# Optimization experiments

Hardware: AMD Instinct MI355X
Metric: run time of the kernel (lower is better)

## Reference

```python
import jax, jax.numpy as jnp
import numpy as np

TOPK = 32
N_HEADS = 8
NEG_INF = float('-inf')


def _l2norm(x, axis):
    # torch F.normalize(p=2): x / max(||x||, 1e-12)
    n = jnp.sqrt(jnp.sum(x * x, axis=axis, keepdims=True))
    return x / jnp.maximum(n, 1e-12)


def _topk_attention(q_in, k_in, v_in, Wq, bq, Wk, bk, Wv, bv):
    # shared ExactTopKAttention (dropout = identity in eval)
    N, L, Hd = q_in.shape
    S = k_in.shape[1]
    E = Hd // N_HEADS
    q = (q_in @ Wq + bq).reshape(N, L, N_HEADS, E)
    k = (k_in @ Wk + bk).reshape(N, S, N_HEADS, E)
    v = (v_in @ Wv + bv).reshape(N, S, N_HEADS, E)
    QK = jnp.einsum('nlhe,nshe->nhls', q, k)  # [N,H,L,S]
    kk = min(TOPK, S)
    _, idx = jax.lax.top_k(QK, kk)  # [N,H,L,kk]
    ni = jnp.arange(N)[:, None, None, None]
    hi = jnp.arange(N_HEADS)[None, :, None, None]
    li = jnp.arange(L)[None, None, :, None]
    mask = jnp.full(QK.shape, NEG_INF, QK.dtype).at[ni, hi, li, idx].set(0.0)
    temp = 1.0 / np.sqrt(E)
    A = jax.nn.softmax(temp * (QK + mask), axis=-1)
    V = jnp.einsum('nhls,nshd->nlhd', A, v).reshape(N, L, Hd)
    return V, A


def _attention_pool(x, w_pool, b_pool):
    # softmax-weighted pooling over sequence dim
    logits = jnp.einsum('bld,d->bl', x, w_pool) + b_pool
    a = jax.nn.softmax(logits, axis=-1)
    pooled = jnp.einsum('bl,bld->bd', a, x)
    return pooled, a


def setup_inputs() -> dict:
    key = jax.random.key(0)
    ks = jax.random.split(key, 16)
    B, L, S, H = 16, 2048, 128, 512
    s = 0.02
    return {
        'seqs_emb': jax.random.normal(ks[0], (B, L, H), jnp.float32),
        'smiles_emb': jax.random.normal(ks[1], (B, S, H), jnp.float32),
        'Wq': jax.random.normal(ks[2], (H, H), jnp.float32) * s,
        'bq': jax.random.normal(ks[3], (H,), jnp.float32) * s,
        'Wk': jax.random.normal(ks[4], (H, H), jnp.float32) * s,
        'bk': jax.random.normal(ks[5], (H,), jnp.float32) * s,
        'Wv': jax.random.normal(ks[6], (H, H), jnp.float32) * s,
        'bv': jax.random.normal(ks[7], (H,), jnp.float32) * s,
        'w_pool': jax.random.normal(ks[8], (H,), jnp.float32) * s,
        'b_pool': jnp.zeros((), jnp.float32),
        'W1': jax.random.normal(ks[9], (2 * H, 2 * H), jnp.float32) * s,
        'b1': jax.random.normal(ks[10], (2 * H,), jnp.float32) * s,
        'W2': jax.random.normal(ks[11], (2 * H, H), jnp.float32) * s,
        'b2': jax.random.normal(ks[12], (H,), jnp.float32) * s,
        'W3': jax.random.normal(ks[13], (H, 1), jnp.float32) * s,
        'b3': jnp.zeros((1,), jnp.float32),
    }


def reference(seqs_emb, smiles_emb, Wq, bq, Wk, bk, Wv, bv, w_pool, b_pool,
              W1, b1, W2, b2, W3, b3):
    # F.normalize(..., dim=1): normalize over the sequence dimension (faithful)
    seqs = _l2norm(seqs_emb, axis=1)
    smis = _l2norm(smiles_emb, axis=1)
    # fusion 1: queries = protein, keys/values = drug (shared weights)
    smiles_out, _ = _topk_attention(seqs, smis, smis, Wq, bq, Wk, bk, Wv, bv)
    smiles_pooled, smiles_attn_pool = _attention_pool(smiles_out, w_pool, b_pool)
    # fusion 2: queries = drug, keys/values = protein (same weights)
    seqs_out, _ = _topk_attention(smis, seqs, seqs, Wq, bq, Wk, bk, Wv, bv)
    seqs_pooled, seqs_attn_pool = _attention_pool(seqs_out, w_pool, b_pool)
    emb = jnp.concatenate([smiles_pooled, seqs_pooled], axis=1)
    emb = _l2norm(emb, axis=1)
    h = jax.nn.relu(emb @ W1 + b1)
    h = jax.nn.relu(h @ W2 + b2)
    out = (h @ W3 + b3).squeeze(-1)  # task_type='reg': no sigmoid
    return emb, out, smiles_attn_pool, seqs_attn_pool
```

## Files before the change

### kernel.cpp

```cpp
#include <hip/hip_runtime.h>
#include <cfloat>
#include <cstdint>

#define NC 1536

#define OUT_EMB 0
#define OUT_OUT 16384
#define OUT_A1  16400
#define OUT_A2  49168

#define WS_NRM_S   0u
#define WS_NRM_M   32768u
#define WS_BCAT    360448u
#define WS_LOG1    366592u
#define WS_PP1     505856u
#define WS_EMB     800768u
#define WS_H1      866304u
#define WS_H2      931840u
#define WS_WCT     1048576u
#define WS_SMISNB  2621440u
#define WS_PSMIS   4718592u
#define WS_SEQSOUT 11010048u
#define WS_SEQSNB  15204352u
#define WS_PSEQS   48758784u
#define WS_SMILOUT WS_SEQSNB
#define WS_PART    WS_PSEQS
#define WS_PARTM   (WS_PSEQS + 2097152u)

typedef float f32x4 __attribute__((ext_vector_type(4)));
typedef __bf16 bf16x8 __attribute__((ext_vector_type(8)));
typedef unsigned short u16x8 __attribute__((ext_vector_type(8)));

__device__ __forceinline__ float bf2f(unsigned short h) {
  return __uint_as_float(((unsigned int)h) << 16);
}
__device__ __forceinline__ unsigned short f2bf(float f) {
  unsigned int u = __float_as_uint(f);
  return (unsigned short)((u + 0x7FFFu + ((u >> 16) & 1u)) >> 16);
}
__device__ __forceinline__ void gld16(const unsigned short* g, unsigned short* l) {
  __builtin_amdgcn_global_load_lds(
      (__attribute__((address_space(1))) unsigned int*)(uintptr_t)g,
      (__attribute__((address_space(3))) unsigned int*)l, 16, 0, 0);
}

__device__ __forceinline__ unsigned pos2elem(unsigned m) {
  unsigned lo = __brev(m & 0xFFFFu) >> 16;
  unsigned hi = __brev(m >> 16) >> 16;
  lo = (lo | (lo << 8)) & 0x00FF00FFu;
  lo = (lo | (lo << 4)) & 0x0F0F0F0Fu;
  lo = (lo | (lo << 2)) & 0x33333333u;
  lo = (lo | (lo << 1)) & 0x55555555u;
  hi = (hi | (hi << 8)) & 0x00FF00FFu;
  hi = (hi | (hi << 4)) & 0x0F0F0F0Fu;
  hi = (hi | (hi << 2)) & 0x33333333u;
  hi = (hi | (hi << 1)) & 0x55555555u;
  return lo | (hi << 1);
}

#define TRANSPOSE16(B)                                                                             \
  {                                                                                                \
    unsigned t;                                                                                    \
    t = (B[0] ^ (B[8] >> 8)) & 0x00FF00FFu; B[0] ^= t; B[8] ^= (t << 8);                           \
    t = (B[1] ^ (B[9] >> 8)) & 0x00FF00FFu; B[1] ^= t; B[9] ^= (t << 8);                           \
    t = (B[2] ^ (B[10] >> 8)) & 0x00FF00FFu; B[2] ^= t; B[10] ^= (t << 8);                         \
    t = (B[3] ^ (B[11] >> 8)) & 0x00FF00FFu; B[3] ^= t; B[11] ^= (t << 8);                         \
    t = (B[4] ^ (B[12] >> 8)) & 0x00FF00FFu; B[4] ^= t; B[12] ^= (t << 8);                         \
    t = (B[5] ^ (B[13] >> 8)) & 0x00FF00FFu; B[5] ^= t; B[13] ^= (t << 8);                         \
    t = (B[6] ^ (B[14] >> 8)) & 0x00FF00FFu; B[6] ^= t; B[14] ^= (t << 8);                         \
    t = (B[7] ^ (B[15] >> 8)) & 0x00FF00FFu; B[7] ^= t; B[15] ^= (t << 8);                         \
    t = (B[0] ^ (B[4] >> 4)) & 0x0F0F0F0Fu; B[0] ^= t; B[4] ^= (t << 4);                           \
    t = (B[1] ^ (B[5] >> 4)) & 0x0F0F0F0Fu; B[1] ^= t; B[5] ^= (t << 4);                           \
    t = (B[2] ^ (B[6] >> 4)) & 0x0F0F0F0Fu; B[2] ^= t; B[6] ^= (t << 4);                           \
    t = (B[3] ^ (B[7] >> 4)) & 0x0F0F0F0Fu; B[3] ^= t; B[7] ^= (t << 4);                           \
    t = (B[8] ^ (B[12] >> 4)) & 0x0F0F0F0Fu; B[8] ^= t; B[12] ^= (t << 4);                         \
    t = (B[9] ^ (B[13] >> 4)) & 0x0F0F0F0Fu; B[9] ^= t; B[13] ^= (t << 4);                         \
    t = (B[10] ^ (B[14] >> 4)) & 0x0F0F0F0Fu; B[10] ^= t; B[14] ^= (t << 4);                       \
    t = (B[11] ^ (B[15] >> 4)) & 0x0F0F0F0Fu; B[11] ^= t; B[15] ^= (t << 4);                       \
    t = (B[0] ^ (B[2] >> 2)) & 0x33333333u; B[0] ^= t; B[2] ^= (t << 2);                           \
    t = (B[1] ^ (B[3] >> 2)) & 0x33333333u; B[1] ^= t; B[3] ^= (t << 2);                           \
    t = (B[4] ^ (B[6] >> 2)) & 0x33333333u; B[4] ^= t; B[6] ^= (t << 2);                           \
    t = (B[5] ^ (B[7] >> 2)) & 0x33333333u; B[5] ^= t; B[7] ^= (t << 2);                           \
    t = (B[8] ^ (B[10] >> 2)) & 0x33333333u; B[8] ^= t; B[10] ^= (t << 2);                         \
    t = (B[9] ^ (B[11] >> 2)) & 0x33333333u; B[9] ^= t; B[11] ^= (t << 2);                         \
    t = (B[12] ^ (B[14] >> 2)) & 0x33333333u; B[12] ^= t; B[14] ^= (t << 2);                       \
    t = (B[13] ^ (B[15] >> 2)) & 0x33333333u; B[13] ^= t; B[15] ^= (t << 2);                       \
    t = (B[0] ^ (B[1] >> 1)) & 0x55555555u; B[0] ^= t; B[1] ^= (t << 1);                           \
    t = (B[2] ^ (B[3] >> 1)) & 0x55555555u; B[2] ^= t; B[3] ^= (t << 1);                           \
    t = (B[4] ^ (B[5] >> 1)) & 0x55555555u; B[4] ^= t; B[5] ^= (t << 1);                           \
    t = (B[6] ^ (B[7] >> 1)) & 0x55555555u; B[6] ^= t; B[7] ^= (t << 1);                           \
    t = (B[8] ^ (B[9] >> 1)) & 0x55555555u; B[8] ^= t; B[9] ^= (t << 1);                           \
    t = (B[10] ^ (B[11] >> 1)) & 0x55555555u; B[10] ^= t; B[11] ^= (t << 1);                       \
    t = (B[12] ^ (B[13] >> 1)) & 0x55555555u; B[12] ^= t; B[13] ^= (t << 1);                       \
    t = (B[14] ^ (B[15] >> 1)) & 0x55555555u; B[14] ^= t; B[15] ^= (t << 1);                       \
  }

__global__ __launch_bounds__(128) void knorm_part(const float* __restrict__ seqs, const float* __restrict__ smis,
                                                  float* __restrict__ part_s, float* __restrict__ part_m) {
  int ls = blockIdx.x, b = blockIdx.y, t = threadIdx.x;
  const float* x; float* part; int slab;
  if (ls < 64) { x = seqs; part = part_s + (size_t)(b * 64 + ls) * 512; slab = b * 64 + ls; }
  else { x = smis; part = part_m + (size_t)(b * 4 + (ls - 64)) * 512; slab = b * 4 + (ls - 64); }
  const float* xp = x + (size_t)slab * 32 * 512 + t * 4;
  float ax = 0.f, ay = 0.f, az = 0.f, aw = 0.f;
  for (int l = 0; l < 32; ++l) {
    float4 v = *(const float4*)(xp + (size_t)l * 512);
    ax += v.x * v.x; ay += v.y * v.y; az += v.z * v.z; aw += v.w * v.w;
  }
  float4 r = {ax, ay, az, aw};
  *(float4*)(part + t * 4) = r;
}

__global__ __launch_bounds__(256) void kfinprep(const float* __restrict__ part_s, const float* __restrict__ part_m,
                                                float* __restrict__ nrm_s, float* __restrict__ nrm_m,
                                                const float* __restrict__ Wq, const float* __restrict__ Wk,
                                                const float* __restrict__ Wv, unsigned short* __restrict__ WT,
                                                const float* bq, const float* bk, const float* bv,
                                                float* bcat, float* log1, float* h1pre, float* h2pre) {
  __shared__ float T[32][33];
  int t = threadIdx.x;
  if (blockIdx.x < 64) {
    int bh0 = blockIdx.x;
    const float* part; float* inv; int NS, bh;
    if (bh0 < 32) { part = part_s; inv = nrm_s; NS = 64; bh = bh0; }
    else { part = part_m; inv = nrm_m; NS = 4; bh = bh0 - 32; }
    int b = bh >> 1, col = (bh & 1) * 256 + t;
    float s = 0.f;
    for (int j = 0; j < NS; ++j) s += part[((size_t)(b * NS + j)) * 512 + col];
    inv[(size_t)b * 512 + col] = 1.f / fmaxf(sqrtf(s), 1e-12f);
  } else {
    int id = blockIdx.x - 64;
    int m = id >> 8, r256 = id & 255;
    if (m < 3) {
      int ti = r256 >> 4, tj = r256 & 15;
      const float* W = m == 0 ? Wq : (m == 1 ? Wk : Wv);
      int c = t & 31, r0 = t >> 5;
#pragma unroll
      for (int j = 0; j < 4; ++j) {
        int r = r0 + j * 8;
        T[r][c] = W[(size_t)(ti * 32 + r) * 512 + tj * 32 + c];
      }
      __syncthreads();
#pragma unroll
      for (int j = 0; j < 4; ++j) {
        int r = r0 + j * 8;
        WT[(size_t)(m * 512 + tj * 32 + r) * 512 + ti * 32 + c] = f2bf(T[c][r]);
      }
    } else {
      int i = r256 * 256 + t;
      if (i < 1536) bcat[i] = i < 512 ? bq[i] : (i < 1024 ? bk[i - 512] : bv[i - 1024]);
      else if (i < 34304) log1[i - 1536] = 0.f;
      else if (i < 50688) h1pre[i - 34304] = 0.f;
      else if (i < 58880) h2pre[i - 50688] = 0.f;
    }
  }
}

__global__ __launch_bounds__(256) void kcast(const float* __restrict__ seqs, const float* __restrict__ smis,
                                             const float* __restrict__ nrm_s, const float* __restrict__ nrm_m,
                                             unsigned short* __restrict__ seqs_nb, unsigned short* __restrict__ smis_nb) {
  const float* x; const float* inv; unsigned short* o; int i4, shiftB;
  if (blockIdx.x < 16384) {
    i4 = (blockIdx.x * 256 + threadIdx.x) * 4; x = seqs; inv = nrm_s; o = seqs_nb; shiftB = 20;
  } else {
    i4 = ((blockIdx.x - 16384) * 256 + threadIdx.x) * 4; x = smis; inv = nrm_m; o = smis_nb; shiftB = 16;
  }
  int b = i4 >> shiftB;
  float4 v = *(const float4*)(x + i4);
  float4 nv = *(const float4*)(inv + (b << 9) + (i4 & 511));
  ushort4 r;
  r.x = f2bf(v.x * nv.x); r.y = f2bf(v.y * nv.y);
  r.z = f2bf(v.z * nv.z); r.w = f2bf(v.w * nv.w);
  *(ushort4*)(o + i4) = r;
}

__global__ __launch_bounds__(256) void kgemm(const unsigned short* __restrict__ A1,
                                             const unsigned short* __restrict__ A2,
                                             const unsigned short* __restrict__ Bt,
                                             const float* __restrict__ bias,
                                             unsigned short* __restrict__ C1,
                                             unsigned short* __restrict__ C2) {
  const int K = 512, N = NC, NT = 12;
  __shared__ unsigned short As[2][128 * 32], Bs[2][128 * 32];
  int tid = threadIdx.x, lane = tid & 63, wave = tid >> 6;
  int id = blockIdx.x;
  const unsigned short* A; unsigned short* C;
  if (id < 3072) { A = A1; C = C1; }
  else { A = A2; C = C2; id -= 3072; }
  int xcd = id & 7, j = id >> 3;
  int mloc = j / NT, n = j - mloc * NT;
  int m0 = (mloc * 8 + xcd) * 128, n0 = n * 128;
  f32x4 acc[4][4] = {};
  int wm = (wave >> 1) * 64, wn = (wave & 1) * 64;
  int frow = lane & 15, fk = (lane >> 4) * 8;

  auto stage = [&](int buf, int k0) {
#pragma unroll
    for (int jj = 0; jj < 2; ++jj) {
      int ch = jj * 256 + tid;
      int row = ch >> 2, kc = (ch & 3) * 8;
      gld16(A + (size_t)(m0 + row) * K + k0 + kc, As[buf] + ch * 8);
      gld16(Bt + (size_t)(n0 + row) * K + k0 + kc, Bs[buf] + ch * 8);
    }
  };

  stage(0, 0);
  __syncthreads();
  int nk = K >> 5;
  for (int it = 0; it < nk; ++it) {
    int cur = it & 1;
    if (it + 1 < nk) stage(cur ^ 1, (it + 1) << 5);
    bf16x8 af[4], bfv[4];
#pragma unroll
    for (int mt = 0; mt < 4; ++mt) af[mt] = *(const bf16x8*)&As[cur][(wm + mt * 16 + frow) * 32 + fk];
#pragma unroll
    for (int nt = 0; nt < 4; ++nt) bfv[nt] = *(const bf16x8*)&Bs[cur][(wn + nt * 16 + frow) * 32 + fk];
#pragma unroll
    for (int mt = 0; mt < 4; ++mt)
#pragma unroll
      for (int nt = 0; nt < 4; ++nt)
        acc[mt][nt] = __builtin_amdgcn_mfma_f32_16x16x32_bf16(af[mt], bfv[nt], acc[mt][nt], 0, 0, 0);
    __syncthreads();
  }
  int q = lane >> 4, c15 = lane & 15;
#pragma unroll
  for (int mt = 0; mt < 4; ++mt)
#pragma unroll
    for (int nt = 0; nt < 4; ++nt) {
      int col = n0 + wn + nt * 16 + c15;
      float bv = bias[col];
#pragma unroll
      for (int r = 0; r < 4; ++r) {
        int row = m0 + wm + mt * 16 + q * 4 + r;
        C[(size_t)row * N + col] = f2bf(acc[mt][nt][r] + bv);
      }
    }
}

__global__ __launch_bounds__(256) void kfusion1(const unsigned short* __restrict__ Pseqs,
                                                const unsigned short* __restrict__ Psmis,
                                                const float* __restrict__ wp,
                                                unsigned short* __restrict__ smil,
                                                float* __restrict__ logits) {
  constexpr int PP = 136;
  __shared__ unsigned short Sc[64 * PP];
  __shared__ unsigned short Vt[64 * PP];
  int tid = threadIdx.x, lane = tid & 63, w = tid >> 6;
  int lt = blockIdx.x, h = blockIdx.y, b = blockIdx.z;
  int l0 = lt * 64;
  int frow = lane & 15, q = lane >> 4, fk8 = q * 8;

  for (int ch = tid; ch < 1024; ch += 256) {
    int s = ch >> 3, e8 = (ch & 7) * 8;
    u16x8 vv = *(const u16x8*)&Psmis[(size_t)(b * 128 + s) * NC + 1024 + h * 64 + e8];
#pragma unroll
    for (int j = 0; j < 8; ++j) {
      int e = e8 + j;
      Vt[e * PP + (s ^ (e & 56))] = vv[j];
    }
  }

  {
    f32x4 acc[8] = {};
    const unsigned short* qrow = Pseqs + (size_t)(b * 2048 + l0 + w * 16 + frow) * NC + h * 64 + fk8;
#pragma unroll
    for (int ks = 0; ks < 2; ++ks) {
      bf16x8 a = *(const bf16x8*)(qrow + ks * 32);
#pragma unroll
      for (int nt = 0; nt < 8; ++nt) {
        bf16x8 bb = *(const bf16x8*)&Psmis[(size_t)(b * 128 + nt * 16 + frow) * NC + 512 + h * 64 + ks * 32 + fk8];
        acc[nt] = __builtin_amdgcn_mfma_f32_16x16x32_bf16(a, bb, acc[nt], 0, 0, 0);
      }
    }
#pragma unroll
    for (int nt = 0; nt < 8; ++nt)
#pragma unroll
      for (int r = 0; r < 4; ++r)
        Sc[(w * 16 + q * 4 + r) * PP + nt * 16 + frow] = f2bf(acc[nt][r]);
  }
  __syncthreads();

  {
    int i = lane >> 2, seg = lane & 3;
    int row = w * 16 + i;
    unsigned short* rb = &Sc[row * PP + seg * 32];
    unsigned orig[16], B[16];
#pragma unroll
    for (int jb = 0; jb < 4; ++jb) {
      uint4 qv = *(const uint4*)(rb + jb * 8);
      orig[jb * 4 + 0] = qv.x; orig[jb * 4 + 1] = qv.y;
      orig[jb * 4 + 2] = qv.z; orig[jb * 4 + 3] = qv.w;
    }
#pragma unroll
    for (int j = 0; j < 16; ++j) {
      unsigned s = (orig[j] >> 15) & 0x00010001u;
      B[j] = orig[j] ^ (s * 0x7FFFu) ^ 0x80008000u;
    }
    TRANSPOSE16(B)
    unsigned act = 0xFFFFFFFFu, gt = 0u, Tv = 0u;
    int rem = 32;
#pragma unroll
    for (int bit = 15; bit >= 0; --bit) {
      unsigned bm = B[15 - bit] & act;
      int c = __popc(bm);
      c += __shfl_xor(c, 1);
      c += __shfl_xor(c, 2);
      bool take = (c >= rem);
      act = take ? bm : (act ^ bm);
      gt = take ? gt : (gt | bm);
      rem = take ? rem : (rem - c);
      Tv = take ? (Tv | (1u << bit)) : Tv;
    }
    unsigned hT = (Tv & 0x8000u) ? (Tv ^ 0x8000u) : (Tv ^ 0xFFFFu);
    float vT = bf2f((unsigned short)hT);
    unsigned gtE = pos2elem(gt), actE = pos2elem(act);
    int pc = __popc(actE);
    int pr1 = __shfl_up(pc, 1);
    int inc = pc + ((seg >= 1) ? pr1 : 0);
    int pr2 = __shfl_up(inc, 2);
    inc += ((seg >= 2) ? pr2 : 0);
    int tie_pre = inc - pc;
    int budget = rem - tie_pre;
    budget = budget < 0 ? 0 : (budget > pc ? pc : budget);
    unsigned selT = 0u, m = actE;
    for (int t = 0; t < budget; ++t) { unsigned bb2 = m & (~m + 1u); selT |= bb2; m ^= bb2; }
    unsigned sel = gtE | selT;
    unsigned* wb = (unsigned*)rb;
#pragma unroll
    for (int j = 0; j < 16; ++j) {
      unsigned d = orig[j];
      float v0 = bf2f((unsigned short)(d & 0xFFFFu));
      float v1 = bf2f((unsigned short)(d >> 16));
      float e0 = ((sel >> (2 * j)) & 1u) ? __expf((v0 - vT) * 0.125f) : 0.f;
      float e1 = ((sel >> (2 * j + 1)) & 1u) ? __expf((v1 - vT) * 0.125f) : 0.f;
      wb[j] = (unsigned)f2bf(e0) | ((unsigned)f2bf(e1) << 16);
    }
  }
  __syncthreads();

  f32x4 oacc[4] = {};
  f32x4 dacc = {};
  bf16x8 ones;
#pragma unroll
  for (int j = 0; j < 8; ++j) ones[j] = (__bf16)1.0f;
#pragma unroll
  for (int k0 = 0; k0 < 128; k0 += 32) {
    bf16x8 a = *(const bf16x8*)&Sc[(w * 16 + frow) * PP + k0 + fk8];
#pragma unroll
    for (int nt = 0; nt < 4; ++nt) {
      int e = nt * 16 + frow;
      bf16x8 bb = *(const bf16x8*)&Vt[e * PP + ((k0 + fk8) ^ (e & 56))];
      oacc[nt] = __builtin_amdgcn_mfma_f32_16x16x32_bf16(a, bb, oacc[nt], 0, 0, 0);
    }
    dacc = __builtin_amdgcn_mfma_f32_16x16x32_bf16(a, ones, dacc, 0, 0, 0);
  }
  float inv4[4];
#pragma unroll
  for (int r = 0; r < 4; ++r) inv4[r] = 1.f / dacc[r];
  float wv[4];
#pragma unroll
  for (int nt = 0; nt < 4; ++nt) wv[nt] = wp[h * 64 + nt * 16 + frow];
  float lg[4];
#pragma unroll
  for (int r = 0; r < 4; ++r) lg[r] = 0.f;
#pragma unroll
  for (int nt = 0; nt < 4; ++nt)
#pragma unroll
    for (int r = 0; r < 4; ++r) {
      float ov = oacc[nt][r] * inv4[r];
      smil[(size_t)(b * 2048 + l0 + w * 16 + q * 4 + r) * 512 + h * 64 + nt * 16 + frow] = f2bf(ov);
      lg[r] += ov * wv[nt];
    }
#pragma unroll
  for (int d = 1; d < 16; d <<= 1)
#pragma unroll
    for (int r = 0; r < 4; ++r) lg[r] += __shfl_xor(lg[r], d);
  if (frow == 0) {
#pragma unroll
    for (int r = 0; r < 4; ++r)
      atomicAdd(&logits[b * 2048 + l0 + w * 16 + q * 4 + r], lg[r]);
  }
}

__global__ __launch_bounds__(1024, 8) void kf2fused(const unsigned short* __restrict__ Psmis,
                                                    const unsigned short* __restrict__ Pseqs,
                                                    float* __restrict__ seqs_out) {
  __shared__ unsigned short S[16 * 2048];
  __shared__ float pS[16][32];
  __shared__ int   sS[16][32];
  int tid = threadIdx.x, lane = tid & 63, w = tid >> 6;
  int bh = blockIdx.x, rt = blockIdx.y;
  int b = bh >> 3, h = bh & 7;
  int frow = lane & 15, q = lane >> 4, fk8 = q * 8;

  {
    const unsigned short* qrow = Psmis + (size_t)(b * 128 + rt * 16 + frow) * NC + h * 64 + fk8;
    bf16x8 a0 = *(const bf16x8*)qrow;
    bf16x8 a1 = *(const bf16x8*)(qrow + 32);
    const unsigned short* Bb = Pseqs + (size_t)(b * 2048) * NC + 512 + h * 64 + fk8;
#pragma unroll
    for (int nt = 0; nt < 8; ++nt) {
      int n0 = w * 128 + nt * 16;
      const unsigned short* brow = Bb + (size_t)(n0 + frow) * NC;
      bf16x8 b0 = *(const bf16x8*)brow;
      bf16x8 b1 = *(const bf16x8*)(brow + 32);
      f32x4 acc = {};
      acc = __builtin_amdgcn_mfma_f32_16x16x32_bf16(a0, b0, acc, 0, 0, 0);
      acc = __builtin_amdgcn_mfma_f32_16x16x32_bf16(a1, b1, acc, 0, 0, 0);
      int el = n0 + frow;
      int cc = el >> 3;
      int base = cc ^ ((cc >> 3) & 7);
#pragma unroll
      for (int r = 0; r < 4; ++r) {
        int row = q * 4 + r;
        S[row * 2048 + ((base ^ (row & 7)) << 3) + (el & 7)] = f2bf(acc[r]);
      }
    }
  }
  __syncthreads();

  int lr = w, x = w & 7;

  unsigned B[16];
  {
    const uint4* p4 = (const uint4*)&S[lr * 2048];
#pragma unroll
    for (int i = 0; i < 4; ++i) {
      int cc = lane * 4 + i;
      int base = cc ^ ((cc >> 3) & 7);
      uint4 qa = p4[base ^ x];
      B[i * 4 + 0] = qa.x; B[i * 4 + 1] = qa.y; B[i * 4 + 2] = qa.z; B[i * 4 + 3] = qa.w;
    }
  }
#pragma unroll
  for (int i = 0; i < 16; ++i) {
    unsigned s0 = (B[i] >> 15) & 0x00010001u;
    B[i] = B[i] ^ (s0 * 0x7FFFu) ^ 0x80008000u;
  }
  TRANSPOSE16(B)
  unsigned act = 0xFFFFFFFFu, gt = 0u, Tv = 0u;
  int rem = 32;
#pragma unroll
  for (int bit = 15; bit >= 0; --bit) {
    unsigned bm = B[15 - bit] & act;
    int c = __popc(bm);
#pragma unroll
    for (int d = 1; d < 64; d <<= 1) c += __shfl_xor(c, d);
    bool take = (c >= rem);
    unsigned actx = act ^ bm;
    act = take ? bm : actx;
    gt = take ? gt : (gt | bm);
    rem = take ? rem : (rem - c);
    Tv = take ? (Tv | (1u << bit)) : Tv;
  }
  unsigned hT = (Tv & 0x8000u) ? (Tv ^ 0x8000u) : (Tv ^ 0xFFFFu);
  float vT = bf2f((unsigned short)hT);

  gt = pos2elem(gt);
  act = pos2elem(act);

  int pc_tie = __popc(act);
  int inc = pc_tie;
#pragma unroll
  for (int d = 1; d < 64; d <<= 1) { int y = __shfl_up(inc, d); if (lane >= d) inc += y; }
  int tie_pre = inc - pc_tie;
  int budget = rem - tie_pre;
  budget = budget < 0 ? 0 : (budget > pc_tie ? pc_tie : budget);
  int total_lane = __popc(gt) + budget;
  int inc2 = total_lane;
#pragma unroll
  for (int d = 1; d < 64; d <<= 1) { int y = __shfl_up(inc2, d); if (lane >= d) inc2 += y; }
  int slot = inc2 - total_lane;

  float lsum = 0.f;
  {
    unsigned m = gt;
    while (m) {
      int e = __builtin_ctz(m); m &= m - 1;
      int gidx = (lane << 5) + e;
      int cc = gidx >> 3;
      float v = bf2f(S[lr * 2048 + (((cc ^ ((cc >> 3) & 7)) ^ x) << 3) + (gidx & 7)]);
      float ev = __expf((v - vT) * 0.125f);
      pS[lr][slot] = ev; sS[lr][slot] = gidx; ++slot; lsum += ev;
    }
    m = act;
    for (int taken = 0; taken < budget; ++taken) {
      int e = __builtin_ctz(m); m &= m - 1;
      int gidx = (lane << 5) + e;
      int cc = gidx >> 3;
      float v = bf2f(S[lr * 2048 + (((cc ^ ((cc >> 3) & 7)) ^ x) << 3) + (gidx & 7)]);
      float ev = __expf((v - vT) * 0.125f);
      pS[lr][slot] = ev; sS[lr][slot] = gidx; ++slot; lsum += ev;
    }
  }
  float den = lsum;
#pragma unroll
  for (int d = 1; d < 64; d <<= 1) den += __shfl_xor(den, d);

  float acc = 0.f;
  const unsigned short* Vb = Pseqs + (size_t)(b * 2048) * NC + 1024 + h * 64 + lane;
#pragma unroll 8
  for (int t = 0; t < 32; ++t) {
    acc += pS[lr][t] * bf2f(Vb[(size_t)sS[lr][t] * NC]);
  }
  seqs_out[(size_t)(b * 128 + rt * 16 + lr) * 512 + h * 64 + lane] = acc / den;
}

__global__ __launch_bounds__(256) void kpool1b(const unsigned short* __restrict__ x,
                                               const float* __restrict__ logits,
                                               float* __restrict__ aout, float* __restrict__ pp) {
  __shared__ float red[256];
  __shared__ float aS[256];
  int t = threadIdx.x;
  int b = blockIdx.x >> 4, ls = (blockIdx.x >> 1) & 7, cj = blockIdx.x & 1;
  const float* lg = logits + b * 2048;
  float lm = -FLT_MAX;
  for (int j = t; j < 2048; j += 256) lm = fmaxf(lm, lg[j]);
  red[t] = lm; __syncthreads();
  for (int s = 128; s > 0; s >>= 1) { if (t < s) red[t] = fmaxf(red[t], red[t + s]); __syncthreads(); }
  float M = red[0]; __syncthreads();
  float sm = 0.f;
  for (int j = t; j < 2048; j += 256) sm += __expf(lg[j] - M);
  red[t] = sm; __syncthreads();
  for (int s = 128; s > 0; s >>= 1) { if (t < s) red[t] += red[t + s]; __syncthreads(); }
  float D = red[0];
  int l0 = ls * 256;
  float a = __expf(lg[l0 + t] - M) / D;
  aS[t] = a;
  if (cj == 0) aout[b * 2048 + l0 + t] = a;
  __syncthreads();
  int col = cj * 256 + t;
  float acc0 = 0.f;
  const unsigned short* xb = x + ((size_t)b * 2048 + l0) * 512 + col;
#pragma unroll 8
  for (int ll = 0; ll < 256; ++ll) acc0 += aS[ll] * bf2f(xb[(size_t)ll * 512]);
  pp[(size_t)(b * 8 + ls) * 512 + col] = acc0;
}

__global__ __launch_bounds__(256) void kpool2emb(const float* __restrict__ x,
                                                 const float* __restrict__ wp, const float* __restrict__ bp,
                                                 const float* __restrict__ pp,
                                                 float* __restrict__ a2out, float* __restrict__ embo) {
  __shared__ float lgS[128];
  __shared__ float red[256];
  int t = threadIdx.x, lane = t & 63, wave = t >> 6;
  int b = blockIdx.x;
  for (int i = 0; i < 32; ++i) {
    int row = wave * 32 + i;
    const float* xp = x + (size_t)(b * 128 + row) * 512;
    float acc = 0.f;
#pragma unroll
    for (int j = 0; j < 8; ++j) acc += xp[lane + 64 * j] * wp[lane + 64 * j];
#pragma unroll
    for (int d = 1; d < 64; d <<= 1) acc += __shfl_xor(acc, d);
    if (lane == 0) lgS[row] = acc + bp[0];
  }
  __syncthreads();
  if (wave == 0) {
    float a0 = lgS[lane], a1 = lgS[64 + lane];
    float m = fmaxf(a0, a1);
#pragma unroll
    for (int d = 1; d < 64; d <<= 1) m = fmaxf(m, __shfl_xor(m, d));
    float e0 = __expf(a0 - m), e1 = __expf(a1 - m);
    float sden = e0 + e1;
#pragma unroll
    for (int d = 1; d < 64; d <<= 1) sden += __shfl_xor(sden, d);
    a0 = e0 / sden; a1 = e1 / sden;
    lgS[lane] = a0; lgS[64 + lane] = a1;
    a2out[b * 128 + lane] = a0;
    a2out[b * 128 + 64 + lane] = a1;
  }
  __syncthreads();
  float acc0 = 0.f, acc1 = 0.f;
#pragma unroll 4
  for (int row = 0; row < 128; ++row) {
    float av = lgS[row];
    const float* xp = x + (size_t)(b * 128 + row) * 512;
    acc0 += av * xp[t];
    acc1 += av * xp[t + 256];
  }
  float pre0 = 0.f, pre1 = 0.f;
  for (int lsl = 0; lsl < 8; ++lsl) {
    pre0 += pp[(size_t)(b * 8 + lsl) * 512 + t];
    pre1 += pp[(size_t)(b * 8 + lsl) * 512 + 256 + t];
  }
  float ssq = pre0 * pre0 + pre1 * pre1 + acc0 * acc0 + acc1 * acc1;
  red[t] = ssq; __syncthreads();
  for (int s2 = 128; s2 > 0; s2 >>= 1) { if (t < s2) red[t] += red[t + s2]; __syncthreads(); }
  float inv = 1.f / fmaxf(sqrtf(red[0]), 1e-12f);
  embo[(size_t)b * 1024 + t] = pre0 * inv;
  embo[(size_t)b * 1024 + 256 + t] = pre1 * inv;
  embo[(size_t)b * 1024 + 512 + t] = acc0 * inv;
  embo[(size_t)b * 1024 + 768 + t] = acc1 * inv;
}

__global__ __launch_bounds__(256) void kh1(const float* __restrict__ emb, const float* __restrict__ W1,
                                           float* __restrict__ h1pre) {
  __shared__ float eS[4][64];
  int t = threadIdx.x;
  int jc = blockIdx.x, bg = blockIdx.y, kc = blockIdx.z;
  int j = jc * 256 + t, b0 = bg * 4, i0 = kc * 64;
  eS[t >> 6][t & 63] = emb[(size_t)(b0 + (t >> 6)) * 1024 + i0 + (t & 63)];
  __syncthreads();
  float a0 = 0.f, a1 = 0.f, a2 = 0.f, a3 = 0.f;
#pragma unroll 8
  for (int i = 0; i < 64; ++i) {
    float w = W1[(size_t)(i0 + i) * 1024 + j];
    a0 += eS[0][i] * w; a1 += eS[1][i] * w; a2 += eS[2][i] * w; a3 += eS[3][i] * w;
  }
  atomicAdd(&h1pre[(b0 + 0) * 1024 + j], a0);
  atomicAdd(&h1pre[(b0 + 1) * 1024 + j], a1);
  atomicAdd(&h1pre[(b0 + 2) * 1024 + j], a2);
  atomicAdd(&h1pre[(b0 + 3) * 1024 + j], a3);
}

__global__ __launch_bounds__(256) void kh2(const float* __restrict__ h1pre, const float* __restrict__ b1,
                                           const float* __restrict__ W2, float* __restrict__ h2pre) {
  __shared__ float eS[4][64];
  int t = threadIdx.x;
  int jc = blockIdx.x, bg = blockIdx.y, kc = blockIdx.z;
  int j = jc * 256 + t, b0 = bg * 4, i0 = kc * 64;
  eS[t >> 6][t & 63] = fmaxf(h1pre[(size_t)(b0 + (t >> 6)) * 1024 + i0 + (t & 63)] + b1[i0 + (t & 63)], 0.f);
  __syncthreads();
  float a0 = 0.f, a1 = 0.f, a2 = 0.f, a3 = 0.f;
#pragma unroll 8
  for (int i = 0; i < 64; ++i) {
    float w = W2[(size_t)(i0 + i) * 512 + j];
    a0 += eS[0][i] * w; a1 += eS[1][i] * w; a2 += eS[2][i] * w; a3 += eS[3][i] * w;
  }
  atomicAdd(&h2pre[(b0 + 0) * 512 + j], a0);
  atomicAdd(&h2pre[(b0 + 1) * 512 + j], a1);
  atomicAdd(&h2pre[(b0 + 2) * 512 + j], a2);
  atomicAdd(&h2pre[(b0 + 3) * 512 + j], a3);
}

__global__ __launch_bounds__(256) void kout(const float* __restrict__ h2pre, const float* __restrict__ b2,
                                            const float* __restrict__ W3, const float* __restrict__ b3,
                                            float* __restrict__ outp) {
  __shared__ float red[256];
  int t = threadIdx.x, b = blockIdx.x;
  float acc = 0.f;
  for (int j = t; j < 512; j += 256)
    acc += fmaxf(h2pre[b * 512 + j] + b2[j], 0.f) * W3[j];
  red[t] = acc; __syncthreads();
  for (int s = 128; s > 0; s >>= 1) { if (t < s) red[t] += red[t + s]; __syncthreads(); }
  if (t == 0) outp[b] = red[0] + b3[0];
}

extern "C" void kernel_launch(void* const* d_in, const int* in_sizes, int n_in,
                              void* d_out, int out_size, void* d_ws, size_t ws_size,
                              hipStream_t stream) {
  const float* seqs = (const float*)d_in[0];
  const float* smis = (const float*)d_in[1];
  const float* Wq = (const float*)d_in[2];
  const float* bq = (const float*)d_in[3];
  const float* Wk = (const float*)d_in[4];
  const float* bk = (const float*)d_in[5];
  const float* Wv = (const float*)d_in[6];
  const float* bv = (const float*)d_in[7];
  const float* wp = (const float*)d_in[8];
  const float* bp = (const float*)d_in[9];
  const float* W1 = (const float*)d_in[10];
  const float* b1 = (const float*)d_in[11];
  const float* W2 = (const float*)d_in[12];
  const float* b2 = (const float*)d_in[13];
  const float* W3 = (const float*)d_in[14];
  const float* b3 = (const float*)d_in[15];
  float* out = (float*)d_out;
  char* ws = (char*)d_ws;

  float* nrm_s = (float*)(ws + WS_NRM_S);
  float* nrm_m = (float*)(ws + WS_NRM_M);
  float* part_s = (float*)(ws + WS_PART);
  float* part_m = (float*)(ws + WS_PARTM);
  float* bcat = (float*)(ws + WS_BCAT);
  float* log1 = (float*)(ws + WS_LOG1);
  float* pp1 = (float*)(ws + WS_PP1);
  float* h1pre = (float*)(ws + WS_H1);
  float* h2pre = (float*)(ws + WS_H2);
  unsigned short* wct = (unsigned short*)(ws + WS_WCT);
  unsigned short* smis_nb = (unsigned short*)(ws + WS_SMISNB);
  unsigned short* Psmis = (unsigned short*)(ws + WS_PSMIS);
  float* seqs_out = (float*)(ws + WS_SEQSOUT);
  unsigned short* seqs_nb = (unsigned short*)(ws + WS_SEQSNB);
  unsigned short* Pseqs = (unsigned short*)(ws + WS_PSEQS);
  unsigned short* smil = (unsigned short*)(ws + WS_SMILOUT);

  knorm_part<<<dim3(68, 16), 128, 0, stream>>>(seqs, smis, part_s, part_m);
  kfinprep<<<dim3(1088), 256, 0, stream>>>(part_s, part_m, nrm_s, nrm_m,
                                           Wq, Wk, Wv, wct, bq, bk, bv, bcat, log1, h1pre, h2pre);
  kcast<<<dim3(17408), 256, 0, stream>>>(seqs, smis, nrm_s, nrm_m, seqs_nb, smis_nb);
  kgemm<<<dim3(3264), 256, 0, stream>>>(seqs_nb, smis_nb, wct, bcat, Pseqs, Psmis);
  kfusion1<<<dim3(32, 8, 16), 256, 0, stream>>>(Pseqs, Psmis, wp, smil, log1);
  kpool1b<<<dim3(256), 256, 0, stream>>>(smil, log1, out + OUT_A1, pp1);
  kf2fused<<<dim3(128, 8), 1024, 0, stream>>>(Psmis, Pseqs, seqs_out);
  kpool2emb<<<dim3(16), 256, 0, stream>>>(seqs_out, wp, bp, pp1, out + OUT_A2, out + OUT_EMB);
  kh1<<<dim3(4, 4, 16), 256, 0, stream>>>(out + OUT_EMB, W1, h1pre);
  kh2<<<dim3(2, 4, 16), 256, 0, stream>>>(h1pre, b1, W2, h2pre);
  kout<<<dim3(16), 256, 0, stream>>>(h2pre, b2, W3, b3, out + OUT_OUT);
}
```

Baseline: 396.6 us.

## Merge pool1 into fusion-2 launch and fold MLP head into cooperative kernel

```diff
diff --git a/kernel.cpp b/kernel.cpp
--- a/kernel.cpp
+++ b/kernel.cpp
@@ -1,6 +1,9 @@
 #include <hip/hip_runtime.h>
+#include <hip/hip_cooperative_groups.h>
 #include <cfloat>
 #include <cstdint>
+
+namespace cg = cooperative_groups;
 
 #define NC 1536
 
@@ -382,14 +385,52 @@
   }
 }
 
-__global__ __launch_bounds__(1024, 8) void kf2fused(const unsigned short* __restrict__ Psmis,
-                                                    const unsigned short* __restrict__ Pseqs,
-                                                    float* __restrict__ seqs_out) {
+__global__ __launch_bounds__(1024, 8) void kf2pool(const unsigned short* __restrict__ Psmis,
+                                                   const unsigned short* __restrict__ Pseqs,
+                                                   float* __restrict__ seqs_out,
+                                                   const unsigned short* __restrict__ xsm,
+                                                   const float* __restrict__ logits,
+                                                   float* __restrict__ aout, float* __restrict__ pp) {
   __shared__ unsigned short S[16 * 2048];
   __shared__ float pS[16][32];
   __shared__ int   sS[16][32];
   int tid = threadIdx.x, lane = tid & 63, w = tid >> 6;
-  int bh = blockIdx.x, rt = blockIdx.y;
+
+  if (blockIdx.x >= 1024) {
+    int bid = blockIdx.x - 1024;
+    int b = bid >> 4, ls = (bid >> 1) & 7, cj = bid & 1;
+    float* redf = (float*)S;
+    float* aSf = (float*)(S + 2048);
+    const float* lg = logits + b * 2048;
+    int t = tid;
+    float lm = fmaxf(lg[t], lg[t + 1024]);
+    redf[t] = lm; __syncthreads();
+    for (int s = 512; s > 0; s >>= 1) { if (t < s) redf[t] = fmaxf(redf[t], redf[t + s]); __syncthreads(); }
+    float M = redf[0]; __syncthreads();
+    float sm = __expf(lg[t] - M) + __expf(lg[t + 1024] - M);
+    redf[t] = sm; __syncthreads();
+    for (int s = 512; s > 0; s >>= 1) { if (t < s) redf[t] += redf[t + s]; __syncthreads(); }
+    float D = redf[0]; __syncthreads();
+    int l0 = ls * 256;
+    int tc = t & 255, g = t >> 8;
+    if (g == 0) {
+      float a = __expf(lg[l0 + tc] - M) / D;
+      aSf[tc] = a;
+      if (cj == 0) aout[b * 2048 + l0 + tc] = a;
+    }
+    __syncthreads();
+    int col = cj * 256 + tc;
+    float acc0 = 0.f;
+    const unsigned short* xb = xsm + ((size_t)b * 2048 + l0 + g * 64) * 512 + col;
+#pragma unroll 8
+    for (int ll = 0; ll < 64; ++ll) acc0 += aSf[g * 64 + ll] * bf2f(xb[(size_t)ll * 512]);
+    redf[t] = acc0; __syncthreads();
+    if (g == 0)
+      pp[(size_t)(b * 8 + ls) * 512 + col] = redf[tc] + redf[256 + tc] + redf[512 + tc] + redf[768 + tc];
+    return;
+  }
+
+  int bh = blockIdx.x & 127, rt = blockIdx.x >> 7;
   int b = bh >> 3, h = bh & 7;
   int frow = lane & 15, q = lane >> 4, fk8 = q * 8;
 
@@ -506,145 +547,122 @@
   seqs_out[(size_t)(b * 128 + rt * 16 + lr) * 512 + h * 64 + lane] = acc / den;
 }
 
-__global__ __launch_bounds__(256) void kpool1b(const unsigned short* __restrict__ x,
-                                               const float* __restrict__ logits,
-                                               float* __restrict__ aout, float* __restrict__ pp) {
-  __shared__ float red[256];
-  __shared__ float aS[256];
-  int t = threadIdx.x;
-  int b = blockIdx.x >> 4, ls = (blockIdx.x >> 1) & 7, cj = blockIdx.x & 1;
-  const float* lg = logits + b * 2048;
-  float lm = -FLT_MAX;
-  for (int j = t; j < 2048; j += 256) lm = fmaxf(lm, lg[j]);
-  red[t] = lm; __syncthreads();
-  for (int s = 128; s > 0; s >>= 1) { if (t < s) red[t] = fmaxf(red[t], red[t + s]); __syncthreads(); }
-  float M = red[0]; __syncthreads();
-  float sm = 0.f;
-  for (int j = t; j < 2048; j += 256) sm += __expf(lg[j] - M);
-  red[t] = sm; __syncthreads();
-  for (int s = 128; s > 0; s >>= 1) { if (t < s) red[t] += red[t + s]; __syncthreads(); }
-  float D = red[0];
-  int l0 = ls * 256;
-  float a = __expf(lg[l0 + t] - M) / D;
-  aS[t] = a;
-  if (cj == 0) aout[b * 2048 + l0 + t] = a;
-  __syncthreads();
-  int col = cj * 256 + t;
-  float acc0 = 0.f;
-  const unsigned short* xb = x + ((size_t)b * 2048 + l0) * 512 + col;
-#pragma unroll 8
-  for (int ll = 0; ll < 256; ++ll) acc0 += aS[ll] * bf2f(xb[(size_t)ll * 512]);
-  pp[(size_t)(b * 8 + ls) * 512 + col] = acc0;
-}
-
-__global__ __launch_bounds__(256) void kpool2emb(const float* __restrict__ x,
-                                                 const float* __restrict__ wp, const float* __restrict__ bp,
-                                                 const float* __restrict__ pp,
-                                                 float* __restrict__ a2out, float* __restrict__ embo) {
+__global__ __launch_bounds__(256) void khead(const float* __restrict__ x,
+                                             const float* __restrict__ wp, const float* __restrict__ bp,
+                                             const float* __restrict__ pp,
+                                             float* __restrict__ a2out, float* __restrict__ embo,
+                                             const float* __restrict__ W1, const float* __restrict__ b1,
+                                             float* __restrict__ h1pre,
+                                             const float* __restrict__ W2, const float* __restrict__ b2,
+                                             float* __restrict__ h2pre,
+                                             const float* __restrict__ W3, const float* __restrict__ b3,
+                                             float* __restrict__ outp) {
+  cg::grid_group grid = cg::this_grid();
   __shared__ float lgS[128];
   __shared__ float red[256];
-  int t = threadIdx.x, lane = t & 63, wave = t >> 6;
-  int b = blockIdx.x;
-  for (int i = 0; i < 32; ++i) {
-    int row = wave * 32 + i;
-    const float* xp = x + (size_t)(b * 128 + row) * 512;
+  __shared__ float eS[4][64];
+  int t = threadIdx.x, bid = blockIdx.x;
+
+  if (bid < 16) {
+    int lane = t & 63, wave = t >> 6, b = bid;
+    for (int i = 0; i < 32; ++i) {
+      int row = wave * 32 + i;
+      const float* xp = x + (size_t)(b * 128 + row) * 512;
+      float acc = 0.f;
+#pragma unroll
+      for (int j = 0; j < 8; ++j) acc += xp[lane + 64 * j] * wp[lane + 64 * j];
+#pragma unroll
+      for (int d = 1; d < 64; d <<= 1) acc += __shfl_xor(acc, d);
+      if (lane == 0) lgS[row] = acc + bp[0];
+    }
+    __syncthreads();
+    if (wave == 0) {
+      float a0 = lgS[lane], a1 = lgS[64 + lane];
+      float m = fmaxf(a0, a1);
+#pragma unroll
+      for (int d = 1; d < 64; d <<= 1) m = fmaxf(m, __shfl_xor(m, d));
+      float e0 = __expf(a0 - m), e1 = __expf(a1 - m);
+      float sden = e0 + e1;
+#pragma unroll
+      for (int d = 1; d < 64; d <<= 1) sden += __shfl_xor(sden, d);
+      a0 = e0 / sden; a1 = e1 / sden;
+      lgS[lane] = a0; lgS[64 + lane] = a1;
+      a2out[b * 128 + lane] = a0;
+      a2out[b * 128 + 64 + lane] = a1;
+    }
+    __syncthreads();
+    float acc0 = 0.f, acc1 = 0.f;
+#pragma unroll 4
+    for (int row = 0; row < 128; ++row) {
+      float av = lgS[row];
+      const float* xp = x + (size_t)(b * 128 + row) * 512;
+      acc0 += av * xp[t];
+      acc1 += av * xp[t + 256];
+    }
+    float pre0 = 0.f, pre1 = 0.f;
+    for (int lsl = 0; lsl < 8; ++lsl) {
+      pre0 += pp[(size_t)(b * 8 + lsl) * 512 + t];
+      pre1 += pp[(size_t)(b * 8 + lsl) * 512 + 256 + t];
+    }
+    float ssq = pre0 * pre0 + pre1 * pre1 + acc0 * acc0 + acc1 * acc1;
+    red[t] = ssq; __syncthreads();
+    for (int s2 = 128; s2 > 0; s2 >>= 1) { if (t < s2) red[t] += red[t + s2]; __syncthreads(); }
+    float inv = 1.f / fmaxf(sqrtf(red[0]), 1e-12f);
+    embo[(size_t)b * 1024 + t] = pre0 * inv;
+    embo[(size_t)b * 1024 + 256 + t] = pre1 * inv;
+    embo[(size_t)b * 1024 + 512 + t] = acc0 * inv;
+    embo[(size_t)b * 1024 + 768 + t] = acc1 * inv;
+  }
+  __threadfence();
+  grid.sync();
+
+  {
+    int jc = bid & 3, bg = (bid >> 2) & 3, kc = bid >> 4;
+    int j = jc * 256 + t, b0 = bg * 4, i0 = kc * 64;
+    eS[t >> 6][t & 63] = embo[(size_t)(b0 + (t >> 6)) * 1024 + i0 + (t & 63)];
+    __syncthreads();
+    float a0 = 0.f, a1 = 0.f, a2 = 0.f, a3 = 0.f;
+#pragma unroll 8
+    for (int i = 0; i < 64; ++i) {
+      float wv = W1[(size_t)(i0 + i) * 1024 + j];
+      a0 += eS[0][i] * wv; a1 += eS[1][i] * wv; a2 += eS[2][i] * wv; a3 += eS[3][i] * wv;
+    }
+    atomicAdd(&h1pre[(b0 + 0) * 1024 + j], a0);
+    atomicAdd(&h1pre[(b0 + 1) * 1024 + j], a1);
+    atomicAdd(&h1pre[(b0 + 2) * 1024 + j], a2);
+    atomicAdd(&h1pre[(b0 + 3) * 1024 + j], a3);
+  }
+  __threadfence();
+  grid.sync();
+
+  if (bid < 128) {
+    int jc = bid & 1, bg = (bid >> 1) & 3, kc = bid >> 3;
+    int j = jc * 256 + t, b0 = bg * 4, i0 = kc * 64;
+    eS[t >> 6][t & 63] = fmaxf(h1pre[(size_t)(b0 + (t >> 6)) * 1024 + i0 + (t & 63)] + b1[i0 + (t & 63)], 0.f);
+    __syncthreads();
+    float a0 = 0.f, a1 = 0.f, a2 = 0.f, a3 = 0.f;
+#pragma unroll 8
+    for (int i = 0; i < 64; ++i) {
+      float wv = W2[(size_t)(i0 + i) * 512 + j];
+      a0 += eS[0][i] * wv; a1 += eS[1][i] * wv; a2 += eS[2][i] * wv; a3 += eS[3][i] * wv;
+    }
+    atomicAdd(&h2pre[(b0 + 0) * 512 + j], a0);
+    atomicAdd(&h2pre[(b0 + 1) * 512 + j], a1);
+    atomicAdd(&h2pre[(b0 + 2) * 512 + j], a2);
+    atomicAdd(&h2pre[(b0 + 3) * 512 + j], a3);
+  }
+  __threadfence();
+  grid.sync();
+
+  if (bid < 16) {
+    int b = bid;
     float acc = 0.f;
-#pragma unroll
-    for (int j = 0; j < 8; ++j) acc += xp[lane + 64 * j] * wp[lane + 64 * j];
-#pragma unroll
-    for (int d = 1; d < 64; d <<= 1) acc += __shfl_xor(acc, d);
-    if (lane == 0) lgS[row] = acc + bp[0];
-  }
-  __syncthreads();
-  if (wave == 0) {
-    float a0 = lgS[lane], a1 = lgS[64 + lane];
-    float m = fmaxf(a0, a1);
-#pragma unroll
-    for (int d = 1; d < 64; d <<= 1) m = fmaxf(m, __shfl_xor(m, d));
-    float e0 = __expf(a0 - m), e1 = __expf(a1 - m);
-    float sden = e0 + e1;
-#pragma unroll
-    for (int d = 1; d < 64; d <<= 1) sden += __shfl_xor(sden, d);
-    a0 = e0 / sden; a1 = e1 / sden;
-    lgS[lane] = a0; lgS[64 + lane] = a1;
-    a2out[b * 128 + lane] = a0;
-    a2out[b * 128 + 64 + lane] = a1;
-  }
-  __syncthreads();
-  float acc0 = 0.f, acc1 = 0.f;
-#pragma unroll 4
-  for (int row = 0; row < 128; ++row) {
-    float av = lgS[row];
-    const float* xp = x + (size_t)(b * 128 + row) * 512;
-    acc0 += av * xp[t];
-    acc1 += av * xp[t + 256];
-  }
-  float pre0 = 0.f, pre1 = 0.f;
-  for (int lsl = 0; lsl < 8; ++lsl) {
-    pre0 += pp[(size_t)(b * 8 + lsl) * 512 + t];
-    pre1 += pp[(size_t)(b * 8 + lsl) * 512 + 256 + t];
-  }
-  float ssq = pre0 * pre0 + pre1 * pre1 + acc0 * acc0 + acc1 * acc1;
-  red[t] = ssq; __syncthreads();
-  for (int s2 = 128; s2 > 0; s2 >>= 1) { if (t < s2) red[t] += red[t + s2]; __syncthreads(); }
-  float inv = 1.f / fmaxf(sqrtf(red[0]), 1e-12f);
-  embo[(size_t)b * 1024 + t] = pre0 * inv;
-  embo[(size_t)b * 1024 + 256 + t] = pre1 * inv;
-  embo[(size_t)b * 1024 + 512 + t] = acc0 * inv;
-  embo[(size_t)b * 1024 + 768 + t] = acc1 * inv;
-}
-
-__global__ __launch_bounds__(256) void kh1(const float* __restrict__ emb, const float* __restrict__ W1,
-                                           float* __restrict__ h1pre) {
-  __shared__ float eS[4][64];
-  int t = threadIdx.x;
-  int jc = blockIdx.x, bg = blockIdx.y, kc = blockIdx.z;
-  int j = jc * 256 + t, b0 = bg * 4, i0 = kc * 64;
-  eS[t >> 6][t & 63] = emb[(size_t)(b0 + (t >> 6)) * 1024 + i0 + (t & 63)];
-  __syncthreads();
-  float a0 = 0.f, a1 = 0.f, a2 = 0.f, a3 = 0.f;
-#pragma unroll 8
-  for (int i = 0; i < 64; ++i) {
-    float w = W1[(size_t)(i0 + i) * 1024 + j];
-    a0 += eS[0][i] * w; a1 += eS[1][i] * w; a2 += eS[2][i] * w; a3 += eS[3][i] * w;
-  }
-  atomicAdd(&h1pre[(b0 + 0) * 1024 + j], a0);
-  atomicAdd(&h1pre[(b0 + 1) * 1024 + j], a1);
-  atomicAdd(&h1pre[(b0 + 2) * 1024 + j], a2);
-  atomicAdd(&h1pre[(b0 + 3) * 1024 + j], a3);
-}
-
-__global__ __launch_bounds__(256) void kh2(const float* __restrict__ h1pre, const float* __restrict__ b1,
-                                           const float* __restrict__ W2, float* __restrict__ h2pre) {
-  __shared__ float eS[4][64];
-  int t = threadIdx.x;
-  int jc = blockIdx.x, bg = blockIdx.y, kc = blockIdx.z;
-  int j = jc * 256 + t, b0 = bg * 4, i0 = kc * 64;
-  eS[t >> 6][t & 63] = fmaxf(h1pre[(size_t)(b0 + (t >> 6)) * 1024 + i0 + (t & 63)] + b1[i0 + (t & 63)], 0.f);
-  __syncthreads();
-  float a0 = 0.f, a1 = 0.f, a2 = 0.f, a3 = 0.f;
-#pragma unroll 8
-  for (int i = 0; i < 64; ++i) {
-    float w = W2[(size_t)(i0 + i) * 512 + j];
-    a0 += eS[0][i] * w; a1 += eS[1][i] * w; a2 += eS[2][i] * w; a3 += eS[3][i] * w;
-  }
-  atomicAdd(&h2pre[(b0 + 0) * 512 + j], a0);
-  atomicAdd(&h2pre[(b0 + 1) * 512 + j], a1);
-  atomicAdd(&h2pre[(b0 + 2) * 512 + j], a2);
-  atomicAdd(&h2pre[(b0 + 3) * 512 + j], a3);
-}
-
-__global__ __launch_bounds__(256) void kout(const float* __restrict__ h2pre, const float* __restrict__ b2,
-                                            const float* __restrict__ W3, const float* __restrict__ b3,
-                                            float* __restrict__ outp) {
-  __shared__ float red[256];
-  int t = threadIdx.x, b = blockIdx.x;
-  float acc = 0.f;
-  for (int j = t; j < 512; j += 256)
-    acc += fmaxf(h2pre[b * 512 + j] + b2[j], 0.f) * W3[j];
-  red[t] = acc; __syncthreads();
-  for (int s = 128; s > 0; s >>= 1) { if (t < s) red[t] += red[t + s]; __syncthreads(); }
-  if (t == 0) outp[b] = red[0] + b3[0];
+    for (int j = t; j < 512; j += 256)
+      acc += fmaxf(h2pre[b * 512 + j] + b2[j], 0.f) * W3[j];
+    red[t] = acc; __syncthreads();
+    for (int s = 128; s > 0; s >>= 1) { if (t < s) red[t] += red[t + s]; __syncthreads(); }
+    if (t == 0) outp[b] = red[0] + b3[0];
+  }
 }
 
 extern "C" void kernel_launch(void* const* d_in, const int* in_sizes, int n_in,
@@ -692,10 +710,16 @@
   kcast<<<dim3(17408), 256, 0, stream>>>(seqs, smis, nrm_s, nrm_m, seqs_nb, smis_nb);
   kgemm<<<dim3(3264), 256, 0, stream>>>(seqs_nb, smis_nb, wct, bcat, Pseqs, Psmis);
   kfusion1<<<dim3(32, 8, 16), 256, 0, stream>>>(Pseqs, Psmis, wp, smil, log1);
-  kpool1b<<<dim3(256), 256, 0, stream>>>(smil, log1, out + OUT_A1, pp1);
-  kf2fused<<<dim3(128, 8), 1024, 0, stream>>>(Psmis, Pseqs, seqs_out);
-  kpool2emb<<<dim3(16), 256, 0, stream>>>(seqs_out, wp, bp, pp1, out + OUT_A2, out + OUT_EMB);
-  kh1<<<dim3(4, 4, 16), 256, 0, stream>>>(out + OUT_EMB, W1, h1pre);
-  kh2<<<dim3(2, 4, 16), 256, 0, stream>>>(h1pre, b1, W2, h2pre);
-  kout<<<dim3(16), 256, 0, stream>>>(h2pre, b2, W3, b3, out + OUT_OUT);
-}
+  kf2pool<<<dim3(1280), 1024, 0, stream>>>(Psmis, Pseqs, seqs_out, smil, log1, out + OUT_A1, pp1);
+  {
+    float* a2outp = out + OUT_A2;
+    float* embop = out + OUT_EMB;
+    float* outp = out + OUT_OUT;
+    void* args[] = {(void*)&seqs_out, (void*)&wp, (void*)&bp, (void*)&pp1,
+                    (void*)&a2outp, (void*)&embop,
+                    (void*)&W1, (void*)&b1, (void*)&h1pre,
+                    (void*)&W2, (void*)&b2, (void*)&h2pre,
+                    (void*)&W3, (void*)&b3, (void*)&outp};
+    hipLaunchCooperativeKernel((const void*)khead, dim3(256), dim3(256), args, 0, stream);
+  }
+}
```

After: 557.7 us. 1.41x slower.
